# Performance work log

Measured on AMD Instinct MI355X. Metric: run time of the kernel, lower is better.

The kernel has to match this reference:

```python
import jax, jax.numpy as jnp
import numpy as np

B, N, IN_DIM, OUT = 4, 4096, 3, 40
NPTS = [1024, 256, 64, 16]   # base_points // sampling_ratio
K, FIRST_K = 8, 16
EPS = 1e-5

def gelu(t):
    return jax.nn.gelu(t, approximate=False)  # torch nn.GELU default (erf)

def pdist2(a, b):
    # a: (b,d,m), b: (b,d,n) -> squared pairwise distances (b,m,n)
    aa = jnp.sum(a * a, axis=1)[:, :, None]
    bb = jnp.sum(b * b, axis=1)[:, None, :]
    return aa + bb - 2.0 * jnp.einsum('bdm,bdn->bmn', a, b)

def knn_idx(a, b, k):
    # indices of k nearest points of b for each point of a
    return jax.lax.top_k(-pdist2(a, b), k)[1]

def gather_nbr(x, ind):
    # x: (b,d,n), ind: (b,m,k) -> (b,d,m,k)
    b, d, n = x.shape
    m, k = ind.shape[1], ind.shape[2]
    idx = jnp.broadcast_to(ind.reshape(b, 1, m * k), (b, d, m * k))
    return jnp.take_along_axis(x, idx, axis=2).reshape(b, d, m, k)

def bn(x):
    # BatchNorm (training-mode batch stats, gamma=1, beta=0 as at init)
    ax = (0,) + tuple(range(2, x.ndim))
    mu = jnp.mean(x, axis=ax, keepdims=True)
    var = jnp.mean((x - mu) ** 2, axis=ax, keepdims=True)
    return (x - mu) / jnp.sqrt(var + EPS)

def route(x, nbr):
    # (b,d,n),(b,n,k) -> (b,2d,n,k) : cat([neighbor - center, center])
    sel = gather_nbr(x, nbr)
    xc = x[:, :, :, None]
    return jnp.concatenate([sel - xc, jnp.broadcast_to(xc, sel.shape)], axis=1)

def edge_conv(x, l1, l2, sc, k, nbr=None):
    if nbr is None:
        nbr = knn_idx(x, x, k)  # dynamic graph in feature space
    h = jnp.max(jnp.einsum('of,bfnk->bonk', l1, route(x, nbr)), axis=-1)
    h = gelu(bn(h))
    h = jnp.max(jnp.einsum('of,bfnk->bonk', l2, route(h, nbr)), axis=-1)
    short = x if sc is None else jnp.einsum('of,bfn->bon', sc, x)
    return gelu(bn(short + h))

def fps(xyz, m):
    # farthest point sampling; xyz: (b,3,n) -> indices (b,m); start index 0
    pts = jnp.transpose(xyz, (0, 2, 1))  # (b,n,3)
    b, n, _ = pts.shape
    def body(carry, _):
        dmin, last = carry
        lp = jnp.take_along_axis(pts, last[:, None, None], axis=1)  # (b,1,3)
        d = jnp.sum((pts - lp) ** 2, axis=-1)
        dmin = jnp.minimum(dmin, d)
        nxt = jnp.argmax(dmin, axis=-1).astype(jnp.int32)
        return (dmin, nxt), last
    init = (jnp.full((b, n), jnp.inf, pts.dtype), jnp.zeros((b,), jnp.int32))
    _, inds = jax.lax.scan(body, init, None, length=m)
    return jnp.transpose(inds)  # (b,m)

def _forward(x, xyz, mlp_w, mlp_b, c0_l1, c0_l2, l1s, l2s, scs,
             head_w1, head_w2, head_b2):
    b = x.shape[0]
    nbr0 = knn_idx(xyz, xyz, FIRST_K)
    h = gelu(bn(jnp.einsum('oi,bin->bon', mlp_w, x) + mlp_b[None, :, None]))
    h = edge_conv(h, c0_l1, c0_l2, None, FIRST_K, nbr=nbr0)
    cur = xyz
    for i in range(4):
        m = NPTS[i]
        sind = fps(cur, m)
        sxyz = jnp.take_along_axis(
            cur, jnp.broadcast_to(sind[:, None, :], (b, cur.shape[1], m)), axis=2)
        nbr = knn_idx(sxyz, cur, K)
        cur = jnp.mean(gather_nbr(cur, nbr), axis=-1)      # sampled xyz = nbr mean
        h = jnp.max(gather_nbr(h, nbr), axis=-1)           # sampled feat = nbr max
        h = edge_conv(h, l1s[i], l2s[i], scs[i], K)
    g = jnp.mean(h, axis=-1)                               # global average pool
    g = gelu(bn(g @ head_w1.T))
    return g @ head_w2.T + head_b2[None, :]


def setup_inputs() -> dict:
    key = jax.random.key(0)
    ks = jax.random.split(key, 20)
    def w(k, o, i):
        return (jax.random.normal(k, (o, i), jnp.float32) / np.sqrt(i)).astype(jnp.float32)
    return {
        'x': jax.random.normal(ks[0], (B, IN_DIM, N), jnp.float32),
        'xyz': jax.random.normal(ks[1], (B, 3, N), jnp.float32),
        'mlp_w': w(ks[2], 64, IN_DIM), 'mlp_b': jnp.zeros((64,), jnp.float32),
        'c0_l1': w(ks[3], 64, 128), 'c0_l2': w(ks[4], 64, 128),
        's0_l1': w(ks[5], 64, 128), 's0_l2': w(ks[6], 64, 128),
        's1_l1': w(ks[7], 128, 128), 's1_l2': w(ks[8], 128, 256), 's1_sc': w(ks[9], 128, 64),
        's2_l1': w(ks[10], 256, 256), 's2_l2': w(ks[11], 256, 512), 's2_sc': w(ks[12], 256, 128),
        's3_l1': w(ks[13], 512, 512), 's3_l2': w(ks[14], 512, 1024), 's3_sc': w(ks[15], 512, 256),
        'head_w1': w(ks[16], 256, 512), 'head_w2': w(ks[17], OUT, 256),
        'head_b2': jnp.zeros((OUT,), jnp.float32),
    }


def reference(x, xyz, mlp_w, mlp_b, c0_l1, c0_l2, s0_l1, s0_l2,
              s1_l1, s1_l2, s1_sc, s2_l1, s2_l2, s2_sc, s3_l1, s3_l2, s3_sc,
              head_w1, head_w2, head_b2):
    return _forward(x, xyz, mlp_w, mlp_b, c0_l1, c0_l2,
                    (s0_l1, s1_l1, s2_l1, s3_l1),
                    (s0_l2, s1_l2, s2_l2, s3_l2),
                    (None, s1_sc, s2_sc, s3_sc),
                    head_w1, head_w2, head_b2)
```

## Files before the change

kernel.cpp:

```cpp
#include <hip/hip_runtime.h>
#include <math.h>

#define NCHUNK 32
typedef unsigned long long ull;

__device__ __forceinline__ float gelu_f(float v){
  return 0.5f*v*(1.0f+erff(v*0.70710678118654752440f));
}

__device__ __forceinline__ unsigned flipf(float d){
  unsigned u = __float_as_uint(d);
  return (u & 0x80000000u) ? ~u : (u | 0x80000000u);
}

template<int CTRL>
__device__ __forceinline__ ull dpp64(ull k){
  int lo = __builtin_amdgcn_update_dpp(0, (int)(unsigned)k,       CTRL, 0xF, 0xF, true);
  int hi = __builtin_amdgcn_update_dpp(0, (int)(unsigned)(k>>32), CTRL, 0xF, 0xF, true);
  return ((ull)(unsigned)hi<<32) | (unsigned)lo;
}
__device__ __forceinline__ ull rl64(ull k, int l){
  unsigned lo = (unsigned)__builtin_amdgcn_readlane((int)(unsigned)k, l);
  unsigned hi = (unsigned)__builtin_amdgcn_readlane((int)(unsigned)(k>>32), l);
  return ((ull)hi<<32) | lo;
}
__device__ __forceinline__ ull fmax64(ull a, ull b){
  return (ull)__double_as_longlong(fmax(__longlong_as_double((long long)a),
                                        __longlong_as_double((long long)b)));
}
__device__ __forceinline__ ull wave_fmax(ull k){
  k = fmax64(k, dpp64<0xB1>(k));
  k = fmax64(k, dpp64<0x4E>(k));
  k = fmax64(k, dpp64<0x141>(k));
  k = fmax64(k, dpp64<0x140>(k));
  ull a=rl64(k,0), b=rl64(k,16), c=rl64(k,32), d=rl64(k,48);
  return fmax64(fmax64(a,b), fmax64(c,d));
}
template<int CTRL>
__device__ __forceinline__ double dmin_dpp(double k){
  ull o = dpp64<CTRL>((ull)__double_as_longlong(k));
  return fmin(k, __longlong_as_double((long long)o));
}
__device__ __forceinline__ double wave_dmin(double k){
  k = dmin_dpp<0xB1>(k);
  k = dmin_dpp<0x4E>(k);
  k = dmin_dpp<0x141>(k);
  k = dmin_dpp<0x140>(k);
  ull kb = (ull)__double_as_longlong(k);
  double a = __longlong_as_double((long long)rl64(kb,0));
  double b = __longlong_as_double((long long)rl64(kb,16));
  double c = __longlong_as_double((long long)rl64(kb,32));
  double d = __longlong_as_double((long long)rl64(kb,48));
  return fmin(fmin(a,b), fmin(c,d));
}


template<int K, int T>
__device__ __forceinline__ void knn_body(
    const float* __restrict__ cand, int n,
    const float* __restrict__ qsrc, const int* __restrict__ qidx, int m,
    int* __restrict__ nbr, float* __restrict__ outc,
    int b, int qblk, int qoff, char* smem)
{
  float4* tile = (float4*)smem;
  constexpr int NWV = T/64;
  int wv = threadIdx.x >> 6, lane = threadIdx.x & 63;
  int q = qblk*NWV + wv + qoff;
  const float* cb = cand + (size_t)b*3*n;
  int qi = qidx ? qidx[(size_t)b*m + q] : q;
  const float* qb = qsrc + (size_t)b*3*n;
  float qx = qb[qi], qy = qb[n+qi], qz = qb[2*n+qi];
  float aa = (qx*qx + qy*qy) + qz*qz;

  double a[K];
  #pragma unroll
  for (int k=0;k<K;k++) a[k] = 1e300;

  for (int base=0; base<n; base+=1024){
    int cnt = min(1024, n-base);
    for (int j=threadIdx.x; j<cnt; j+=T){
      float x=cb[base+j], y=cb[n+base+j], z=cb[2*n+base+j];
      tile[j] = make_float4(x,y,z,(x*x+y*y)+z*z);
    }
    __syncthreads();
    int steps = cnt >> 6;
    double jd = (double)(base + lane);
    for (int i=0;i<steps;i++){
      int j = lane + (i<<6);
      float4 c = tile[j];
      float d = aa + c.w - 2.0f*((qx*c.x+qy*c.y)+qz*c.z);
      double key = (double)flipf(d) * 4096.0 + jd;
      if (key < a[K-1]){
        #pragma unroll
        for (int k=K-1;k>=1;k--)
          a[k] = fmin(fmax(a[k-1], key), a[k]);
        a[0] = fmin(a[0], key);
      }
      jd += 64.0;
    }
    __syncthreads();
  }

  double head = a[0];
  int res[K];
  #pragma unroll
  for (int r=0; r<K; r++){
    double mk = wave_dmin(head);
    res[r] = (int)((ull)mk & 4095u);
    if (head == mk){
      #pragma unroll
      for (int i2=0;i2<K-1;i2++) a[i2]=a[i2+1];
      a[K-1] = 1e300;
      head = a[0];
    }
  }
  if (lane == 0){
    int* o = nbr + ((size_t)b*m + q)*K;
    #pragma unroll
    for (int r=0;r<K;r++) o[r] = res[r];
  }
  if (outc != nullptr && lane < 3){
    const float* cd = cb + (size_t)lane*n;
    float s=0;
    #pragma unroll
    for (int k=0;k<K;k++) s += cd[res[k]];
    outc[((size_t)b*3 + lane)*m + q] = s * (1.0f/K);
  }
}

template<int K>
__device__ __forceinline__ void topk_body(
    const float* __restrict__ G, const float* __restrict__ aa, int m,
    int* __restrict__ nbr, int b, int qblk, char* smem)
{
  float* abs_s = (float*)smem;
  int wv = threadIdx.x >> 6, lane = threadIdx.x & 63;
  int q = qblk*4 + wv;
  const float* ab = aa + (size_t)b*m;
  for (int j=threadIdx.x; j<m; j+=256) abs_s[j] = ab[j];
  __syncthreads();
  float aq = ab[q];
  const float* Gq = G + ((size_t)b*m + q)*m;

  double a[K];
  #pragma unroll
  for (int k=0;k<K;k++) a[k] = 1e300;

  int steps = (m+63)>>6;
  double jd = (double)lane;
  for (int i=0;i<steps;i++){
    int j = lane + (i<<6);
    double key = 1e300;
    if (j < m){
      float g = Gq[j];
      float d = aq + abs_s[j] - 2.0f*g;
      key = (double)flipf(d) * 4096.0 + jd;
    }
    if (key < a[K-1]){
      #pragma unroll
      for (int k=K-1;k>=1;k--)
        a[k] = fmin(fmax(a[k-1], key), a[k]);
      a[0] = fmin(a[0], key);
    }
    jd += 64.0;
  }
  double head = a[0];
  int res[K];
  #pragma unroll
  for (int r=0; r<K; r++){
    double mk = wave_dmin(head);
    res[r] = (int)((ull)mk & 4095u);
    if (head == mk){
      #pragma unroll
      for (int i2=0;i2<K-1;i2++) a[i2]=a[i2+1];
      a[K-1] = 1e300;
      head = a[0];
    }
  }
  if (lane == 0){
    int* o = nbr + ((size_t)b*m + q)*K;
    #pragma unroll
    for (int r=0;r<K;r++) o[r] = res[r];
  }
}

template<int NP, int T, int M>
__device__ __forceinline__ void fps_mw_seg(const float* __restrict__ cur, int n,
                                           int* __restrict__ sind, float* __restrict__ gdmin,
                                           int b, int M0, int M1, char* smem)
{
  constexpr int NW = T/64;
  int tid = threadIdx.x;
  int wv = tid>>6;
  const float* cb = cur + (size_t)b*3*n;
  float4* lp = (float4*)smem;
  ull* wred = (ull*)(smem + sizeof(float4)*NP*T);
  float* gd = gdmin + (size_t)b*n;
  float px[NP], py[NP], pz[NP], dmin[NP];
  unsigned nj[NP];
  #pragma unroll
  for (int s=0;s<NP;s++){
    int j = tid + s*T;
    px[s]=cb[j]; py[s]=cb[n+j]; pz[s]=cb[2*n+j];
    dmin[s] = (M0==0) ? 1e30f : gd[j];
    nj[s] = (unsigned)(~j);
    lp[j] = make_float4(px[s],py[s],pz[s],0.f);
  }
  __syncthreads();
  int ci = (M0==0) ? 0 : sind[(size_t)b*M + (M0-1)];
  float4 w0 = lp[ci];
  float X = w0.x, Y = w0.y, Z = w0.z;
  if (M0==0 && tid==0) sind[(size_t)b*M] = 0;
  __builtin_amdgcn_s_setprio(3);
  int p = 0;
  int s0 = (M0==0) ? 1 : M0;
  for (int step=s0; step<M1; step++){
    ull key[NP];
    #pragma unroll
    for (int s=0;s<NP;s++){
      float dx=px[s]-X, dy=py[s]-Y, dz=pz[s]-Z;
      float d = (dx*dx + dy*dy) + dz*dz;
      float nd = fminf(dmin[s], d);
      dmin[s] = nd;
      key[s] = ((ull)__float_as_uint(nd)<<32) | nj[s];
    }
    #pragma unroll
    for (int w=NP; w>1; w>>=1)
      #pragma unroll
      for (int i=0;i<NP;i++) if (i < (w>>1))
        key[i] = fmax64(key[i], key[i+(w>>1)]);
    ull wk = wave_fmax(key[0]);
    if ((tid&63)==0) wred[p*NW + wv] = wk;
    __syncthreads();
    const ulonglong2* wp2 = (const ulonglong2*)(wred + p*NW);
    ulonglong2 m0 = wp2[0], m1 = wp2[1], m2 = wp2[2], m3 = wp2[3];
    ull gk = fmax64(fmax64(fmax64(m0.x,m0.y), fmax64(m1.x,m1.y)),
                    fmax64(fmax64(m2.x,m2.y), fmax64(m3.x,m3.y)));
    int gi = (int)(~(unsigned)gk);
    if (tid==0) sind[(size_t)b*M + step] = gi;
    float4 wp = lp[gi];
    X=wp.x; Y=wp.y; Z=wp.z;
    p ^= 1;
  }
  __builtin_amdgcn_s_setprio(0);
  #pragma unroll
  for (int s=0;s<NP;s++) gd[tid + s*T] = dmin[s];
}

template<int NP, int M>
__device__ __forceinline__ void fps_sw_body(const float* __restrict__ cur, int n,
                                            int* __restrict__ sind, int b, char* smem)
{
  int lane = threadIdx.x;
  const float* cb = cur + (size_t)b*3*n;
  float4* lp = (float4*)smem;
  float px[NP], py[NP], pz[NP], dmin[NP];
  unsigned nj[NP];
  #pragma unroll
  for (int s=0;s<NP;s++){
    int j = lane + s*64;
    px[s]=cb[j]; py[s]=cb[n+j]; pz[s]=cb[2*n+j]; dmin[s]=1e30f;
    nj[s] = (unsigned)(~j);
    lp[j] = make_float4(px[s],py[s],pz[s],0.f);
  }
  float X = lp[0].x, Y = lp[0].y, Z = lp[0].z;
  if (lane==0) sind[(size_t)b*M] = 0;
  __builtin_amdgcn_s_setprio(3);
  for (int step=1; step<M; step++){
    ull key[NP];
    #pragma unroll
    for (int s=0;s<NP;s++){
      float dx=px[s]-X, dy=py[s]-Y, dz=pz[s]-Z;
      float d = (dx*dx + dy*dy) + dz*dz;
      float nd = fminf(dmin[s], d);
      dmin[s] = nd;
      key[s] = ((ull)__float_as_uint(nd)<<32) | nj[s];
    }
    #pragma unroll
    for (int w=NP; w>1; w>>=1)
      #pragma unroll
      for (int i=0;i<NP;i++) if (i < (w>>1))
        key[i] = fmax64(key[i], key[i+(w>>1)]);
    ull gk = wave_fmax(key[0]);
    int gi = (int)(~(unsigned)gk);
    if (lane==0) sind[(size_t)b*M + step] = gi;
    float4 wp = lp[gi];
    X=wp.x; Y=wp.y; Z=wp.z;
  }
  __builtin_amdgcn_s_setprio(0);
}

template<int NP, int M>
__device__ __forceinline__ void fps_sw_seg(const float* __restrict__ cur, int n,
                                           int* __restrict__ sind, float* __restrict__ gdmin,
                                           int b, int M0, int M1, char* smem)
{
  int lane = threadIdx.x;
  const float* cb = cur + (size_t)b*3*n;
  float4* lp = (float4*)smem;
  float* gd = gdmin + (size_t)b*n;
  float px[NP], py[NP], pz[NP], dmin[NP];
  unsigned nj[NP];
  #pragma unroll
  for (int s=0;s<NP;s++){
    int j = lane + s*64;
    px[s]=cb[j]; py[s]=cb[n+j]; pz[s]=cb[2*n+j];
    dmin[s] = (M0==0) ? 1e30f : gd[j];
    nj[s] = (unsigned)(~j);
    lp[j] = make_float4(px[s],py[s],pz[s],0.f);
  }
  int ci = (M0==0) ? 0 : sind[(size_t)b*M + (M0-1)];
  float4 w0 = lp[ci];
  float X = w0.x, Y = w0.y, Z = w0.z;
  if (M0==0 && lane==0) sind[(size_t)b*M] = 0;
  __builtin_amdgcn_s_setprio(3);
  int s0 = (M0==0) ? 1 : M0;
  for (int step=s0; step<M1; step++){
    ull key[NP];
    #pragma unroll
    for (int s=0;s<NP;s++){
      float dx=px[s]-X, dy=py[s]-Y, dz=pz[s]-Z;
      float d = (dx*dx + dy*dy) + dz*dz;
      float nd = fminf(dmin[s], d);
      dmin[s] = nd;
      key[s] = ((ull)__float_as_uint(nd)<<32) | nj[s];
    }
    #pragma unroll
    for (int w=NP; w>1; w>>=1)
      #pragma unroll
      for (int i=0;i<NP;i++) if (i < (w>>1))
        key[i] = fmax64(key[i], key[i+(w>>1)]);
    ull gk = wave_fmax(key[0]);
    int gi = (int)(~(unsigned)gk);
    if (lane==0) sind[(size_t)b*M + step] = gi;
    float4 wp = lp[gi];
    X=wp.x; Y=wp.y; Z=wp.z;
  }
  __builtin_amdgcn_s_setprio(0);
  #pragma unroll
  for (int s=0;s<NP;s++) gd[lane + s*64] = dmin[s];
}

template<bool DUAL, bool BN>
__device__ __forceinline__ void gemm_body(
    const float* __restrict__ A, const float* __restrict__ B,
    float* __restrict__ out0, float* __restrict__ out1,
    int M, int N, int Kd, int lda, int ldb, int ldo, int boff,
    long sA, long sB, long sO, const float* __restrict__ part, float invR,
    int bxi, int byi, int bzi, char* smem)
{
  A += (size_t)bzi * sA; B += (size_t)bzi * sB;
  float* o0 = out0 + (size_t)bzi * sO;
  float* o1 = DUAL ? (out1 + (size_t)bzi * sO) : nullptr;
  int rowBase = byi*64, colBase = bxi*64;
  float (*As)[64]  = (float(*)[64])smem;
  float (*Bs0)[64] = (float(*)[64])(smem + 4096);
  float (*Bs1)[64] = (float(*)[64])(smem + 8192);
  float* mu_s = (float*)(smem + 12288);
  float* var_s = mu_s + 512;
  int tid = threadIdx.x;
  if (BN){
    for (int oo=tid; oo<Kd; oo+=blockDim.x){
      float s=0, q=0;
      #pragma unroll 4
      for (int c=0;c<NCHUNK;c++){
        s += part[(size_t)c*1024 + oo];
        q += part[(size_t)(NCHUNK+c)*1024 + oo];
      }
      float mu = s*invR;
      mu_s[oo] = mu;
      var_s[oo] = q*invR - mu*mu;
    }
    __syncthreads();
  }
  int ty = tid>>4, tx = tid&15;
  float acc0[4][4] = {}, acc1[4][4] = {};
  int lr = tid>>2, lk = (tid&3)*4;
  for (int k0=0; k0<Kd; k0+=16) {
    float4 va = make_float4(0,0,0,0);
    int r = rowBase + lr;
    if (r < M) va = *(const float4*)(A + (size_t)r*lda + k0 + lk);
    if (BN){
      int c = k0 + lk;
      va.x = gelu_f((va.x - mu_s[c+0]) / sqrtf(var_s[c+0] + 1e-5f));
      va.y = gelu_f((va.y - mu_s[c+1]) / sqrtf(var_s[c+1] + 1e-5f));
      va.z = gelu_f((va.z - mu_s[c+2]) / sqrtf(var_s[c+2] + 1e-5f));
      va.w = gelu_f((va.w - mu_s[c+3]) / sqrtf(var_s[c+3] + 1e-5f));
    }
    As[lk+0][lr]=va.x; As[lk+1][lr]=va.y; As[lk+2][lr]=va.z; As[lk+3][lr]=va.w;
    float4 vb = make_float4(0,0,0,0), vb2 = make_float4(0,0,0,0);
    int c2 = colBase + lr;
    if (c2 < N) {
      vb = *(const float4*)(B + (size_t)c2*ldb + k0 + lk);
      if (DUAL) vb2 = *(const float4*)(B + (size_t)c2*ldb + boff + k0 + lk);
    }
    Bs0[lk+0][lr]=vb.x; Bs0[lk+1][lr]=vb.y; Bs0[lk+2][lr]=vb.z; Bs0[lk+3][lr]=vb.w;
    if (DUAL) {
      Bs1[lk+0][lr]=vb2.x-vb.x; Bs1[lk+1][lr]=vb2.y-vb.y;
      Bs1[lk+2][lr]=vb2.z-vb.z; Bs1[lk+3][lr]=vb2.w-vb.w;
    }
    __syncthreads();
    #pragma unroll
    for (int kk=0;kk<16;kk++){
      float4 a  = *(const float4*)&As[kk][ty*4];
      float4 b0 = *(const float4*)&Bs0[kk][tx*4];
      float av[4]={a.x,a.y,a.z,a.w};
      float b0v[4]={b0.x,b0.y,b0.z,b0.w};
      #pragma unroll
      for (int i=0;i<4;i++)
        #pragma unroll
        for (int j=0;j<4;j++) acc0[i][j] = fmaf(av[i], b0v[j], acc0[i][j]);
      if (DUAL) {
        float4 b1 = *(const float4*)&Bs1[kk][tx*4];
        float b1v[4]={b1.x,b1.y,b1.z,b1.w};
        #pragma unroll
        for (int i=0;i<4;i++)
          #pragma unroll
          for (int j=0;j<4;j++) acc1[i][j] = fmaf(av[i], b1v[j], acc1[i][j]);
      }
    }
    __syncthreads();
  }
  #pragma unroll
  for (int i=0;i<4;i++){
    int r = rowBase + ty*4 + i;
    if (r < M) {
      #pragma unroll
      for (int j=0;j<4;j++){
        int c = colBase + tx*4 + j;
        if (c < N) {
          o0[(size_t)r*ldo + c] = acc0[i][j];
          if (DUAL) o1[(size_t)r*ldo + c] = acc1[i][j];
        }
      }
    }
  }
}

template<bool DUAL, bool BN>
__device__ __forceinline__ void gemm_body_g(
    const float* __restrict__ A, const float* __restrict__ B,
    float* __restrict__ out0, float* __restrict__ out1,
    int M, int N, int Kd, int lda, int ldb, int ldo, int boff,
    const float* __restrict__ part, float invR,
    int bxi, int byi, char* smem)
{
  int rowBase = byi*64, colBase = bxi*64;
  float (*As)[64]  = (float(*)[64])smem;
  float (*Bs0)[64] = (float(*)[64])(smem + 4096);
  float (*Bs1)[64] = (float(*)[64])(smem + 8192);
  float* mu_s = (float*)(smem + 12288);
  float* var_s = mu_s + 512;
  int tid = threadIdx.x;
  bool act = tid < 256;
  if (BN){
    for (int oo=tid; oo<Kd; oo+=blockDim.x){
      float s=0, q=0;
      #pragma unroll 4
      for (int c=0;c<NCHUNK;c++){
        s += part[(size_t)c*1024 + oo];
        q += part[(size_t)(NCHUNK+c)*1024 + oo];
      }
      float mu = s*invR;
      mu_s[oo] = mu;
      var_s[oo] = q*invR - mu*mu;
    }
    __syncthreads();
  }
  int ty = tid>>4, tx = tid&15;
  float acc0[4][4] = {}, acc1[4][4] = {};
  int lr = tid>>2, lk = (tid&3)*4;
  for (int k0=0; k0<Kd; k0+=16) {
    if (act){
      float4 va = make_float4(0,0,0,0);
      int r = rowBase + lr;
      if (r < M) va = *(const float4*)(A + (size_t)r*lda + k0 + lk);
      if (BN){
        int c = k0 + lk;
        va.x = gelu_f((va.x - mu_s[c+0]) / sqrtf(var_s[c+0] + 1e-5f));
        va.y = gelu_f((va.y - mu_s[c+1]) / sqrtf(var_s[c+1] + 1e-5f));
        va.z = gelu_f((va.z - mu_s[c+2]) / sqrtf(var_s[c+2] + 1e-5f));
        va.w = gelu_f((va.w - mu_s[c+3]) / sqrtf(var_s[c+3] + 1e-5f));
      }
      As[lk+0][lr]=va.x; As[lk+1][lr]=va.y; As[lk+2][lr]=va.z; As[lk+3][lr]=va.w;
      float4 vb = make_float4(0,0,0,0), vb2 = make_float4(0,0,0,0);
      int c2 = colBase + lr;
      if (c2 < N) {
        vb = *(const float4*)(B + (size_t)c2*ldb + k0 + lk);
        if (DUAL) vb2 = *(const float4*)(B + (size_t)c2*ldb + boff + k0 + lk);
      }
      Bs0[lk+0][lr]=vb.x; Bs0[lk+1][lr]=vb.y; Bs0[lk+2][lr]=vb.z; Bs0[lk+3][lr]=vb.w;
      if (DUAL) {
        Bs1[lk+0][lr]=vb2.x-vb.x; Bs1[lk+1][lr]=vb2.y-vb.y;
        Bs1[lk+2][lr]=vb2.z-vb.z; Bs1[lk+3][lr]=vb2.w-vb.w;
      }
    }
    __syncthreads();
    if (act){
      #pragma unroll
      for (int kk=0;kk<16;kk++){
        float4 a  = *(const float4*)&As[kk][ty*4];
        float4 b0 = *(const float4*)&Bs0[kk][tx*4];
        float av[4]={a.x,a.y,a.z,a.w};
        float b0v[4]={b0.x,b0.y,b0.z,b0.w};
        #pragma unroll
        for (int i=0;i<4;i++)
          #pragma unroll
          for (int j=0;j<4;j++) acc0[i][j] = fmaf(av[i], b0v[j], acc0[i][j]);
        if (DUAL) {
          float4 b1 = *(const float4*)&Bs1[kk][tx*4];
          float b1v[4]={b1.x,b1.y,b1.z,b1.w};
          #pragma unroll
          for (int i=0;i<4;i++)
            #pragma unroll
            for (int j=0;j<4;j++) acc1[i][j] = fmaf(av[i], b1v[j], acc1[i][j]);
        }
      }
    }
    __syncthreads();
  }
  if (act){
    #pragma unroll
    for (int i=0;i<4;i++){
      int r = rowBase + ty*4 + i;
      if (r < M) {
        #pragma unroll
        for (int j=0;j<4;j++){
          int c = colBase + tx*4 + j;
          if (c < N) {
            out0[(size_t)r*ldo + c] = acc0[i][j];
            if (DUAL) out1[(size_t)r*ldo + c] = acc1[i][j];
          }
        }
      }
    }
  }
}

__device__ __forceinline__ void gather_elem(
    const float* __restrict__ P, const int* __restrict__ nbr,
    const float* __restrict__ addA, const float* __restrict__ addB,
    float* __restrict__ out, int n_out, int n_src, int O, int K, int total, int e)
{
  if (e >= total) return;
  int o = e % O; int r = e / O;
  int b = r / n_out; int i = r % n_out;
  const int* nb = nbr + ((size_t)b*n_out + i)*K;
  float mx = -1e38f;
  for (int k=0;k<K;k++){
    int j = nb[k];
    float v = P[((size_t)b*n_src + j)*O + o];
    mx = fmaxf(mx, v);
  }
  float res = mx;
  if (addA) res += addA[e];
  if (addB) res = addB[e] + res;
  out[e] = res;
}

__device__ __forceinline__ void gatherbn_body(
    const float* __restrict__ P, const int* __restrict__ nbr,
    const float* __restrict__ part, float invR,
    float* __restrict__ out, float* __restrict__ aa,
    int n_out, int n_src, int O, int K, int blk, char* smem)
{
  float* mu_s = (float*)smem; float* var_s = mu_s + 256; float* sv = var_s + 256;
  int tid = threadIdx.x;
  for (int oo=tid; oo<O; oo+=256){
    float s=0, q=0;
    #pragma unroll 4
    for (int c=0;c<NCHUNK;c++){
      s += part[(size_t)c*1024 + oo];
      q += part[(size_t)(NCHUNK+c)*1024 + oo];
    }
    float mu = s*invR;
    mu_s[oo] = mu;
    var_s[oo] = q*invR - mu*mu;
  }
  __syncthreads();
  int e = blk*256 + tid;
  int o = e % O; int r = e / O;
  int b = r / n_out; int i = r % n_out;
  const int* nb = nbr + ((size_t)b*n_out + i)*K;
  float mu = mu_s[o], sd = sqrtf(var_s[o] + 1e-5f);
  float mx = -1e38f;
  for (int k=0;k<K;k++){
    int j = nb[k];
    float p = P[((size_t)b*n_src + j)*O + o];
    float v = gelu_f((p - mu)/sd);
    mx = fmaxf(mx, v);
  }
  out[e] = mx;
  sv[tid] = mx*mx;
  __syncthreads();
  for (int st=O>>1; st>0; st>>=1){
    if (o < st) sv[tid] += sv[tid+st];
    __syncthreads();
  }
  if (o == 0) aa[r] = sv[tid];
}


#define FPS_SMEM 65664

__global__ __launch_bounds__(512,2) void mega1(
    const float* __restrict__ xyz, const float* __restrict__ x,
    const float* __restrict__ mlpw, const float* __restrict__ mlpb,
    int* __restrict__ sind0, float* __restrict__ gdmin,
    int* __restrict__ nbr0, float* __restrict__ hA, int M0, int M1)
{
  __shared__ __align__(16) char SMEM[FPS_SMEM];
  int bid = blockIdx.x;
  if (bid < 4){
    fps_mw_seg<8,512,1024>(xyz, 4096, sind0, gdmin, bid, M0, M1, SMEM);
  } else if (bid < 4+2048){
    int kb = bid - 4;
    knn_body<16,512>(xyz, 4096, xyz, nullptr, 4096, nbr0, nullptr, kb>>9, kb&511, 0, SMEM);
  } else {
    int e = (bid - 2052)*512 + threadIdx.x;
    if (e < 4*4096*64){
      int o = e & 63; int r = e >> 6;
      int b = r / 4096; int i = r % 4096;
      const float* xb = x + (size_t)b*3*4096;
      hA[e] = ((mlpw[o*3+0]*xb[i] + mlpw[o*3+1]*xb[4096+i]) + mlpw[o*3+2]*xb[2*4096+i]) + mlpb[o];
    }
  }
}

__global__ __launch_bounds__(512,2) void fps_bngelu(
    const float* fcur, int* sind, float* gdmin, int M0, int M1,
    float* __restrict__ xx, const float* __restrict__ part, float invR, int O, int total)
{
  __shared__ __align__(16) char SMEM[FPS_SMEM];
  if (blockIdx.x < 4){
    fps_mw_seg<8,512,1024>(fcur, 4096, sind, gdmin, blockIdx.x, M0, M1, SMEM);
    return;
  }
  float* mu_s = (float*)SMEM; float* var_s = mu_s + 512;
  for (int oo=threadIdx.x; oo<O; oo+=512){
    float s=0, q=0;
    #pragma unroll 4
    for (int c=0;c<NCHUNK;c++){
      s += part[(size_t)c*1024 + oo];
      q += part[(size_t)(NCHUNK+c)*1024 + oo];
    }
    float mu = s*invR;
    mu_s[oo] = mu;
    var_s[oo] = q*invR - mu*mu;
  }
  __syncthreads();
  int e = (blockIdx.x-4)*512 + threadIdx.x;
  if (e >= total) return;
  int o = e % O;
  float v = (xx[e]-mu_s[o]) / sqrtf(var_s[o] + 1e-5f);
  xx[e] = gelu_f(v);
}

template<bool DUAL, bool BN>
__global__ __launch_bounds__(512,2) void fps0_gemm(
    const float* fcur, int* sind, float* gdmin, int M0, int M1,
    const float* A, const float* B, float* out0, float* out1,
    int Mg, int Ng, int Kd, int lda, int ldb, int ldo, int boff,
    const float* part, float invR, int nbx)
{
  __shared__ __align__(16) char SMEM[FPS_SMEM];
  if (blockIdx.x < 4){
    fps_mw_seg<8,512,1024>(fcur, 4096, sind, gdmin, blockIdx.x, M0, M1, SMEM);
    return;
  }
  int l = blockIdx.x - 4;
  gemm_body_g<DUAL,BN>(A,B,out0,out1,Mg,Ng,Kd,lda,ldb,ldo,boff,part,invR, l%nbx, l/nbx, SMEM);
}

__global__ __launch_bounds__(512,2) void fps0_gather_knn(
    const float* fcur, int* sind, float* gdmin, int M0, int M1,
    const float* cand, int n, const float* qsrc, const int* qidx, int m,
    int* nbrOut, float* outc, int KNB,
    const float* P, const int* nbr, const float* addA, const float* addB,
    float* out, int n_out, int n_src, int O, int K, int total)
{
  __shared__ __align__(16) char SMEM[FPS_SMEM];
  if (blockIdx.x < 4){
    fps_mw_seg<8,512,1024>(fcur, 4096, sind, gdmin, blockIdx.x, M0, M1, SMEM);
    return;
  }
  int l = blockIdx.x - 4;
  if (l < KNB){
    knn_body<8,512>(cand, n, qsrc, qidx, m, nbrOut, outc, l>>6, l&63, 0, SMEM);
    return;
  }
  int e = (l-KNB)*512 + threadIdx.x;
  gather_elem(P, nbr, addA, addB, out, n_out, n_src, O, K, total, e);
}

__global__ __launch_bounds__(512,2) void fps0_gather(
    const float* fcur, int* sind, float* gdmin, int M0, int M1,
    const float* P, const int* nbr, const float* addA, const float* addB,
    float* out, int n_out, int n_src, int O, int K, int total)
{
  __shared__ __align__(16) char SMEM[FPS_SMEM];
  if (blockIdx.x < 4){
    fps_mw_seg<8,512,1024>(fcur, 4096, sind, gdmin, blockIdx.x, M0, M1, SMEM);
    return;
  }
  int e = (blockIdx.x-4)*512 + threadIdx.x;
  gather_elem(P, nbr, addA, addB, out, n_out, n_src, O, K, total, e);
}

__global__ __launch_bounds__(512,2) void fps0_stats(
    const float* fcur, int* sind, float* gdmin, int M0, int M1,
    const float* __restrict__ x, int R, int O, float* __restrict__ part)
{
  __shared__ __align__(16) char SMEM[FPS_SMEM];
  if (blockIdx.x < 4){
    fps_mw_seg<8,512,1024>(fcur, 4096, sind, gdmin, blockIdx.x, M0, M1, SMEM);
    return;
  }
  int o = threadIdx.x;
  if (o >= O) return;
  int chunk = blockIdx.x - 4;
  int per = (R + NCHUNK - 1)/NCHUNK;
  int r0 = chunk*per, r1 = min(r0+per, R);
  float s=0, q=0;
  for (int r=r0; r<r1; r++){ float v = x[(size_t)r*O + o]; s+=v; q+=v*v; }
  part[(size_t)chunk*1024 + o] = s;
  part[(size_t)(NCHUNK+chunk)*1024 + o] = q;
}

__global__ __launch_bounds__(256) void knn_wave8(
    const float* cand, int n, const float* qsrc, const int* qidx, int m, int qoff,
    int* nbr, float* outc)
{
  __shared__ __align__(16) char SMEM[16384];
  knn_body<8,256>(cand, n, qsrc, qidx, m, nbr, outc, blockIdx.y, blockIdx.x, qoff, SMEM);
}

__global__ __launch_bounds__(256) void fps1_gatherbn(
    const float* fcur, int* sind, float* gdmin, int M0, int M1,
    const float* P, const int* nbr, const float* part, float invR,
    float* out, float* aa, int n_out, int n_src, int O, int K)
{
  __shared__ __align__(16) char SMEM[16384];
  if (blockIdx.x < 4){
    if (threadIdx.x < 64) fps_sw_seg<16,256>(fcur, 1024, sind, gdmin, blockIdx.x, M0, M1, SMEM);
    return;
  }
  gatherbn_body(P, nbr, part, invR, out, aa, n_out, n_src, O, K, blockIdx.x-4, SMEM);
}

__global__ __launch_bounds__(256) void fps1_gram(
    const float* fcur, int* sind, float* gdmin, int M0, int M1,
    const float* Ag, float* outg, int Mg, int Kg, long sAg, long sOg, int ngx, int ngy)
{
  __shared__ __align__(16) char SMEM[16896];
  if (blockIdx.x < 4){
    if (threadIdx.x < 64) fps_sw_seg<16,256>(fcur, 1024, sind, gdmin, blockIdx.x, M0, M1, SMEM);
    return;
  }
  int l = blockIdx.x - 4;
  int bx = l % ngx, by = (l/ngx) % ngy, bz = l/(ngx*ngy);
  gemm_body<false,false>(Ag,Ag,outg,nullptr,Mg,Mg,Kg,Kg,Kg,Mg,0,sAg,sAg,sOg,nullptr,0.f,bx,by,bz,SMEM);
}

__global__ __launch_bounds__(256) void fps1_topk(
    const float* fcur, int* sind, float* gdmin, int M0, int M1,
    const float* G, const float* aa, int m, int* nbr)
{
  __shared__ __align__(16) char SMEM[16384];
  if (blockIdx.x < 4){
    if (threadIdx.x < 64) fps_sw_seg<16,256>(fcur, 1024, sind, gdmin, blockIdx.x, M0, M1, SMEM);
    return;
  }
  int l = blockIdx.x - 4;
  int qpb = m/4;
  topk_body<8>(G, aa, m, nbr, l/qpb, l%qpb, SMEM);
}

template<int NP, int M>
__global__ __launch_bounds__(256) void fps_gather(
    const float* fcur, int fn, int* sind,
    const float* P, const int* nbr, const float* addA, const float* addB,
    float* out, int n_out, int n_src, int O, int K, int total)
{
  __shared__ __align__(16) char SMEM[(NP*64*16 > 4096) ? NP*64*16 : 4096];
  if (blockIdx.x < 4){
    if (threadIdx.x < 64) fps_sw_body<NP,M>(fcur, fn, sind, blockIdx.x, SMEM);
    return;
  }
  gather_elem(P, nbr, addA, addB, out, n_out, n_src, O, K, total, (blockIdx.x-4)*256 + threadIdx.x);
}

template<bool DUAL, bool BN>
__global__ __launch_bounds__(256) void knn_gemm2(
    const float* cand, int n, const float* qsrc, const int* qidx, int m,
    int* nbrOut, float* outc, int KNB,
    const float* A, const float* B, float* out0, float* out1,
    int Mg, int Ng, int Kd, int boff,
    const float* part, float invR, int nbx)
{
  __shared__ __align__(16) char SMEM[16896];
  if (blockIdx.x < KNB){
    int qpb = m/4;
    knn_body<8,256>(cand, n, qsrc, qidx, m, nbrOut, outc, blockIdx.x/qpb, blockIdx.x%qpb, 0, SMEM);
    return;
  }
  int l = blockIdx.x - KNB;
  gemm_body<DUAL,BN>(A,B,out0,out1,Mg,Ng,Kd,Kd,DUAL?2*Kd:Kd,Ng,boff,0,0,0,part,invR, l%nbx, l/nbx, 0, SMEM);
}

__global__ __launch_bounds__(256) void knn_gatherbn(
    const float* cand, int n, const float* qsrc, const int* qidx, int m,
    int* nbrOut, int KNB,
    const float* P, const int* nbr, const float* part, float invR,
    float* out, float* aa, int n_out, int n_src, int O, int K)
{
  __shared__ __align__(16) char SMEM[16384];
  if (blockIdx.x < KNB){
    int qpb = m/4;
    knn_body<8,256>(cand, n, qsrc, qidx, m, nbrOut, nullptr, blockIdx.x/qpb, blockIdx.x%qpb, 0, SMEM);
    return;
  }
  gatherbn_body(P, nbr, part, invR, out, aa, n_out, n_src, O, K, blockIdx.x-KNB, SMEM);
}

__global__ __launch_bounds__(256) void gram_gemm(
    const float* Ag, float* outg, int Mg, int Kg, long sAg, long sOg,
    int ngx, int ngy, int NG,
    const float* A2, const float* B2, float* o20, float* o21,
    int M2, int N2, int K2, int boff2, int nb2x)
{
  __shared__ __align__(16) char SMEM[16896];
  int l = blockIdx.x;
  if (l < NG){
    int bx = l % ngx, by = (l/ngx) % ngy, bz = l/(ngx*ngy);
    gemm_body<false,false>(Ag,Ag,outg,nullptr,Mg,Mg,Kg,Kg,Kg,Mg,0,sAg,sAg,sOg,nullptr,0.f,bx,by,bz,SMEM);
    return;
  }
  l -= NG;
  gemm_body<true,false>(A2,B2,o20,o21,M2,N2,K2,K2,2*K2,N2,boff2,0,0,0,nullptr,0.f, l%nb2x, l/nb2x, 0, SMEM);
}

__global__ __launch_bounds__(256) void gemm2sc(
    const float* A2, const float* B2, float* o20, float* o21, int R, int O2, int O1v,
    const float* part, float invR,
    const float* Asc, const float* Bsc, float* osc, int Cin,
    int nbx, int nby)
{
  __shared__ __align__(16) char SMEM[16896];
  int l = blockIdx.x;
  int half = nbx*nby;
  if (l < half){
    gemm_body<true,true>(A2,B2,o20,o21,R,O2,O1v,O1v,2*O1v,O2,O1v,0,0,0,part,invR, l%nbx, l/nbx, 0, SMEM);
  } else {
    l -= half;
    gemm_body<false,false>(Asc,Bsc,osc,nullptr,R,O2,Cin,Cin,Cin,O2,0,0,0,0,nullptr,0.f, l%nbx, l/nbx, 0, SMEM);
  }
}

__global__ __launch_bounds__(256) void gathermax_kernel(
    const float* P, const int* nbr, const float* addA, const float* addB,
    float* out, int n_out, int n_src, int O, int K, int total)
{
  gather_elem(P, nbr, addA, addB, out, n_out, n_src, O, K, total, blockIdx.x*256 + threadIdx.x);
}

__global__ __launch_bounds__(256) void gatherbn_kernel(
    const float* P, const int* nbr, const float* part, float invR,
    float* out, float* aa, int n_out, int n_src, int O, int K)
{
  __shared__ __align__(16) char SMEM[3072];
  gatherbn_body(P, nbr, part, invR, out, aa, n_out, n_src, O, K, blockIdx.x, SMEM);
}

template<int K>
__global__ __launch_bounds__(256) void topk_wave(
    const float* __restrict__ G, const float* __restrict__ aa, int m,
    int* __restrict__ nbr)
{
  __shared__ __align__(16) char SMEM[4096];
  topk_body<K>(G, aa, m, nbr, blockIdx.y, blockIdx.x, SMEM);
}

__global__ void stats_part_kernel(const float* __restrict__ x, int R, int O,
                                  float* __restrict__ part)
{
  int o = threadIdx.x;
  int chunk = blockIdx.x;
  int per = (R + NCHUNK - 1)/NCHUNK;
  int r0 = chunk*per, r1 = min(r0+per, R);
  float s=0, q=0;
  for (int r=r0; r<r1; r++){ float v = x[(size_t)r*O + o]; s+=v; q+=v*v; }
  part[(size_t)chunk*1024 + o] = s;
  part[(size_t)(NCHUNK+chunk)*1024 + o] = q;
}

__global__ __launch_bounds__(1024) void head_kernel(const float* __restrict__ h,
    const float* __restrict__ part, float invR,
    const float* __restrict__ w1, const float* __restrict__ w2,
    const float* __restrict__ b2, float* __restrict__ out)
{
  __shared__ __align__(16) float mu_s[512], var_s[512];
  __shared__ __align__(16) float g[4*512];
  __shared__ __align__(16) float t[4*256];
  int tid = threadIdx.x;
  for (int oo=tid; oo<512; oo+=1024){
    float s=0, q=0;
    #pragma unroll 4
    for (int c=0;c<NCHUNK;c++){
      s += part[(size_t)c*1024 + oo];
      q += part[(size_t)(NCHUNK+c)*1024 + oo];
    }
    float mu = s*invR;
    mu_s[oo] = mu;
    var_s[oo] = q*invR - mu*mu;
  }
  __syncthreads();
  for (int e=tid; e<2048; e+=1024){
    int b=e>>9, c=e&511;
    float mu = mu_s[c], sd = sqrtf(var_s[c] + 1e-5f);
    float s=0;
    for (int p=0;p<16;p++){
      float v = h[((size_t)(b*16+p))*512 + c];
      s += gelu_f((v-mu)/sd);
    }
    g[e] = s * (1.0f/16.0f);
  }
  __syncthreads();
  {
    int b = tid>>8, j = tid&255;
    const float4* gr = (const float4*)(g + b*512);
    const float4* wr = (const float4*)(w1 + (size_t)j*512);
    float s=0;
    for (int c=0;c<128;c++){
      float4 a=gr[c], w=wr[c];
      s = fmaf(a.x,w.x, fmaf(a.y,w.y, fmaf(a.z,w.z, fmaf(a.w,w.w, s))));
    }
    t[tid] = s;
  }
  __syncthreads();
  if (tid < 256){
    float v0=t[tid], v1=t[256+tid], v2=t[512+tid], v3=t[768+tid];
    float mu = ((v0+v1)+v2+v3)*0.25f;
    float d0=v0-mu, d1=v1-mu, d2=v2-mu, d3=v3-mu;
    float var = ((d0*d0+d1*d1)+d2*d2+d3*d3)*0.25f;
    float sq = sqrtf(var + 1e-5f);
    t[tid]     = gelu_f(d0/sq);
    t[256+tid] = gelu_f(d1/sq);
    t[512+tid] = gelu_f(d2/sq);
    t[768+tid] = gelu_f(d3/sq);
  }
  __syncthreads();
  if (tid < 160){
    int b = tid/40, o = tid%40;
    const float* tr = t + b*256; const float* wr = w2 + (size_t)o*256;
    float s=0;
    for (int j=0;j<256;j++) s = fmaf(tr[j], wr[j], s);
    out[tid] = s + b2[o];
  }
}

extern "C" void kernel_launch(void* const* d_in, const int* in_sizes, int n_in,
                              void* d_out, int out_size, void* d_ws, size_t ws_size,
                              hipStream_t stream)
{
  const float* x    = (const float*)d_in[0];
  const float* xyz  = (const float*)d_in[1];
  const float* mlpw = (const float*)d_in[2];
  const float* mlpb = (const float*)d_in[3];
  const float* c0l1 = (const float*)d_in[4];
  const float* c0l2 = (const float*)d_in[5];
  const float* L1[4] = {(const float*)d_in[6], (const float*)d_in[8],
                        (const float*)d_in[11], (const float*)d_in[14]};
  const float* L2[4] = {(const float*)d_in[7], (const float*)d_in[9],
                        (const float*)d_in[12], (const float*)d_in[15]};
  const float* SC[4] = {nullptr, (const float*)d_in[10],
                        (const float*)d_in[13], (const float*)d_in[16]};
  const float* hw1 = (const float*)d_in[17];
  const float* hw2 = (const float*)d_in[18];
  const float* hb2 = (const float*)d_in[19];
  float* out = (float*)d_out;

  float* ws = (float*)d_ws;
  const size_t MF = 1024*1024;
  float* D    = ws;
  float* hA   = ws + 4*MF;
  float* hX   = ws + 5*MF;
  float* hP   = ws + 6*MF;
  float* hCT  = ws + 7*MF;
  float* hSH  = ws + 8*MF;
  float* hH1  = ws + 9*MF;
  float* hOUT = ws + 10*MF;
  float* aux  = ws + 11*MF;
  int*   nbr0  = (int*)aux;                 aux += 262144;
  int*   nbrS0 = (int*)aux;                 aux += 32768;
  int*   nbrS1 = (int*)aux;                 aux += 8192;
  int*   nbrS2 = (int*)aux;                 aux += 2048;
  int*   nbrS3 = (int*)aux;                 aux += 512;
  int*   nbrF  = (int*)aux;                 aux += 32768;
  int*   sind0 = (int*)aux;                 aux += 4096;
  int*   sind1 = (int*)aux;                 aux += 1024;
  int*   sind2 = (int*)aux;                 aux += 256;
  int*   sind3 = (int*)aux;                 aux += 64;
  float* aa    = aux;                       aux += 4096;
  float* cur1  = aux;                       aux += 12288;
  float* cur2  = aux;                       aux += 3072;
  float* cur3  = aux;                       aux += 768;
  float* part  = aux;                       aux += 65536;
  float* gdmin = aux;                       aux += 16384;

  int tot0 = 4*4096*64;

  mega1<<<4100, 512, 0, stream>>>(xyz, x, mlpw, mlpb, sind0, gdmin, nbr0, hA, 0, 260);
  stats_part_kernel<<<NCHUNK, 64, 0, stream>>>(hA, 16384, 64, part);
  fps_bngelu<<<4+2048, 512, 0, stream>>>(xyz, sind0, gdmin, 260, 390, hA, part, 1.0f/16384.0f, 64, tot0);
  fps0_gemm<true,false><<<4+256, 512, 0, stream>>>(xyz, sind0, gdmin, 390, 517,
      hA, c0l1, hP, hCT, 16384, 64, 64, 64, 128, 64, 64, nullptr, 0.f, 1);
  fps0_gather_knn<<<4+256+2048, 512, 0, stream>>>(xyz, sind0, gdmin, 517, 644,
      xyz, 4096, xyz, sind0, 1024, nbrS0, cur1, 256,
      hP, nbr0, hCT, nullptr, hH1, 4096, 4096, 64, 16, 1048576);
  stats_part_kernel<<<NCHUNK, 64, 0, stream>>>(hH1, 16384, 64, part);
  fps0_gemm<true,true><<<4+256, 512, 0, stream>>>(xyz, sind0, gdmin, 644, 771,
      hH1, c0l2, hP, hCT, 16384, 64, 64, 64, 128, 64, 64, part, 1.0f/16384.0f, 1);
  fps0_gather<<<4+2048, 512, 0, stream>>>(xyz, sind0, gdmin, 771, 898,
      hP, nbr0, hCT, hA, hOUT, 4096, 4096, 64, 16, 1048576);
  fps0_stats<<<4+NCHUNK, 512, 0, stream>>>(xyz, sind0, gdmin, 898, 1024,
      hOUT, 16384, 64, part);

  knn_wave8<<<dim3(128,4),256,0,stream>>>(xyz, 4096, xyz, sind0, 1024, 512, nbrS0, cur1);

  fps1_gatherbn<<<4+1024,256,0,stream>>>(cur1, sind1, gdmin, 0, 86,
      hOUT, nbrS0, part, 1.0f/16384.0f, hX, aa, 1024, 4096, 64, 8);
  fps1_gram<<<4+1024,256,0,stream>>>(cur1, sind1, gdmin, 86, 171,
      hX, D, 1024, 64, (long)1024*64, (long)1024*1024, 16, 16);
  fps1_topk<<<4+1024,256,0,stream>>>(cur1, sind1, gdmin, 171, 256,
      D, aa, 1024, nbrF);
  knn_gemm2<true,false><<<256+64,256,0,stream>>>(cur1, 1024, cur1, sind1, 256,
      nbrS1, cur2, 256,
      hX, L1[0], hP, hCT, 4096, 64, 64, 64, nullptr, 0.f, 1);
  fps_gather<4,64><<<4+1024,256,0,stream>>>(cur2, 256, sind2,
      hP, nbrF, hCT, nullptr, hH1, 1024, 1024, 64, 8, 262144);
  stats_part_kernel<<<NCHUNK, 64, 0, stream>>>(hH1, 4096, 64, part);
  knn_gemm2<true,true><<<64+64,256,0,stream>>>(cur2, 256, cur2, sind2, 64,
      nbrS2, cur3, 64,
      hH1, L2[0], hP, hCT, 4096, 64, 64, 64, part, 1.0f/4096.0f, 1);
  fps_gather<1,16><<<4+1024,256,0,stream>>>(cur3, 64, sind3,
      hP, nbrF, hCT, hX, hA, 1024, 1024, 64, 8, 262144);
  stats_part_kernel<<<NCHUNK, 64, 0, stream>>>(hA, 4096, 64, part);
  knn_gatherbn<<<16+256,256,0,stream>>>(cur3, 64, cur3, sind3, 16,
      nbrS3, 16,
      hA, nbrS1, part, 1.0f/4096.0f, hX, aa, 256, 1024, 64, 8);

  const int   mArr[3]   = {256, 64, 16};
  const int   nsrcArr[3]= {1024, 256, 64};
  const int   CinArr[3] = {64, 128, 256};
  const int   OArr[3]   = {128, 256, 512};
  const int*  nbrSs[3]  = {nbrS1, nbrS2, nbrS3};
  float* hcur = hA;
  float invRprev = 1.0f/4096.0f;
  for (int s=0;s<3;s++){
    int m = mArr[s], nsrc = nsrcArr[s], Cin = CinArr[s], O1 = OArr[s], O2 = OArr[s];
    int R = 4*m;
    int th = R*Cin;
    if (s > 0){
      gatherbn_kernel<<<th/256,256,0,stream>>>(hcur, nbrSs[s], part, invRprev,
                                               hX, aa, m, nsrc, Cin, 8);
    }
    int ngx = (m+63)/64, ngy = (m+63)/64;
    int NG = ngx*ngy*4;
    int nb1x = (O1+63)/64, nb1y = (R+63)/64;
    gram_gemm<<<NG + nb1x*nb1y, 256, 0, stream>>>(
        hX, D, m, Cin, (long)m*Cin, (long)m*m, ngx, ngy, NG,
        hX, L1[s+1], hP, hCT, R, O1, Cin, Cin, nb1x);
    topk_wave<8><<<dim3(m/4,4),256,0,stream>>>(D, aa, m, nbrF);
    int t1 = R*O1;
    gathermax_kernel<<<(t1+255)/256,256,0,stream>>>(hP, nbrF, hCT, nullptr, hH1, m, m, O1, 8, t1);
    stats_part_kernel<<<NCHUNK, O1, 0, stream>>>(hH1, R, O1, part);
    int nbx = (O2+63)/64, nby = (R+63)/64;
    gemm2sc<<<2*nbx*nby,256,0,stream>>>(hH1, L2[s+1], hP, hCT, R, O2, O1, part, 1.0f/R,
                                        hX, SC[s+1], hSH, Cin, nbx, nby);
    int t2 = R*O2;
    float* outbuf = (s&1) ? hA : hOUT;
    gathermax_kernel<<<(t2+255)/256,256,0,stream>>>(hP, nbrF, hCT, hSH, outbuf, m, m, O2, 8, t2);
    stats_part_kernel<<<NCHUNK, O2, 0, stream>>>(outbuf, R, O2, part);
    hcur = outbuf;
    invRprev = 1.0f/R;
  }

  head_kernel<<<1,1024,0,stream>>>(hcur, part, 1.0f/64.0f, hw1, hw2, hb2, out);
}
```

Before: 1.553 ms.

## Spread stage-0 kNN query blocks across FPS-overlapped kernels and split gather-BN

The standalone stage-0 kNN kernel is removed. Its query blocks are spread across the existing FPS-carrying launches: gemm, gather and stats now each run an extra slice of kNN blocks alongside the FPS segment. The FPS iteration ranges per kernel are rebalanced to match. The remaining kNN queries are fused with part of the gather-BN work into a new tail kernel, and fps1_gatherbn handles only the leftover gather-BN blocks. The aim is to fill idle CUs while the serial FPS runs, at the cost of more complex block indexing and a risk of load imbalance.

```diff
diff --git a/kernel.cpp b/kernel.cpp
--- a/kernel.cpp
+++ b/kernel.cpp
@@ -657,8 +657,10 @@
 }
 
 template<bool DUAL, bool BN>
-__global__ __launch_bounds__(512,2) void fps0_gemm(
+__global__ __launch_bounds__(512,2) void fps0_gemm_knn(
     const float* fcur, int* sind, float* gdmin, int M0, int M1,
+    const float* cand, int n, const float* qsrc, const int* qidx, int m,
+    int* nbrOut, float* outc, int qoff, int NQB, int KNB,
     const float* A, const float* B, float* out0, float* out1,
     int Mg, int Ng, int Kd, int lda, int ldb, int ldo, int boff,
     const float* part, float invR, int nbx)
@@ -669,13 +671,18 @@
     return;
   }
   int l = blockIdx.x - 4;
+  if (l < KNB){
+    knn_body<8,512>(cand, n, qsrc, qidx, m, nbrOut, outc, l/NQB, l%NQB, qoff, SMEM);
+    return;
+  }
+  l -= KNB;
   gemm_body_g<DUAL,BN>(A,B,out0,out1,Mg,Ng,Kd,lda,ldb,ldo,boff,part,invR, l%nbx, l/nbx, SMEM);
 }
 
 __global__ __launch_bounds__(512,2) void fps0_gather_knn(
     const float* fcur, int* sind, float* gdmin, int M0, int M1,
     const float* cand, int n, const float* qsrc, const int* qidx, int m,
-    int* nbrOut, float* outc, int KNB,
+    int* nbrOut, float* outc, int qoff, int NQB, int KNB,
     const float* P, const int* nbr, const float* addA, const float* addB,
     float* out, int n_out, int n_src, int O, int K, int total)
 {
@@ -686,39 +693,32 @@
   }
   int l = blockIdx.x - 4;
   if (l < KNB){
-    knn_body<8,512>(cand, n, qsrc, qidx, m, nbrOut, outc, l>>6, l&63, 0, SMEM);
+    knn_body<8,512>(cand, n, qsrc, qidx, m, nbrOut, outc, l/NQB, l%NQB, qoff, SMEM);
     return;
   }
   int e = (l-KNB)*512 + threadIdx.x;
   gather_elem(P, nbr, addA, addB, out, n_out, n_src, O, K, total, e);
 }
 
-__global__ __launch_bounds__(512,2) void fps0_gather(
+__global__ __launch_bounds__(512,2) void fps0_stats_knn(
     const float* fcur, int* sind, float* gdmin, int M0, int M1,
-    const float* P, const int* nbr, const float* addA, const float* addB,
-    float* out, int n_out, int n_src, int O, int K, int total)
+    const float* cand, int n, const float* qsrc, const int* qidx, int m,
+    int* nbrOut, float* outc, int qoff, int NQB, int KNB,
+    const float* __restrict__ x, int R, int O, float* __restrict__ part)
 {
   __shared__ __align__(16) char SMEM[FPS_SMEM];
   if (blockIdx.x < 4){
     fps_mw_seg<8,512,1024>(fcur, 4096, sind, gdmin, blockIdx.x, M0, M1, SMEM);
     return;
   }
-  int e = (blockIdx.x-4)*512 + threadIdx.x;
-  gather_elem(P, nbr, addA, addB, out, n_out, n_src, O, K, total, e);
-}
-
-__global__ __launch_bounds__(512,2) void fps0_stats(
-    const float* fcur, int* sind, float* gdmin, int M0, int M1,
-    const float* __restrict__ x, int R, int O, float* __restrict__ part)
-{
-  __shared__ __align__(16) char SMEM[FPS_SMEM];
-  if (blockIdx.x < 4){
-    fps_mw_seg<8,512,1024>(fcur, 4096, sind, gdmin, blockIdx.x, M0, M1, SMEM);
+  int l = blockIdx.x - 4;
+  if (l < KNB){
+    knn_body<8,512>(cand, n, qsrc, qidx, m, nbrOut, outc, l/NQB, l%NQB, qoff, SMEM);
     return;
   }
   int o = threadIdx.x;
   if (o >= O) return;
-  int chunk = blockIdx.x - 4;
+  int chunk = l - KNB;
   int per = (R + NCHUNK - 1)/NCHUNK;
   int r0 = chunk*per, r1 = min(r0+per, R);
   float s=0, q=0;
@@ -727,12 +727,21 @@
   part[(size_t)(NCHUNK+chunk)*1024 + o] = q;
 }
 
-__global__ __launch_bounds__(256) void knn_wave8(
-    const float* cand, int n, const float* qsrc, const int* qidx, int m, int qoff,
-    int* nbr, float* outc)
+__global__ __launch_bounds__(256) void knn_gatherbn_tail(
+    const float* cand, int n, const float* qsrc, const int* qidx, int m,
+    int* nbrOut, float* outc, int qoff, int NQB, int KNB,
+    const float* P, const int* nbr, const float* part, float invR,
+    float* out, float* aa, int n_out, int n_src, int O, int K)
 {
   __shared__ __align__(16) char SMEM[16384];
-  knn_body<8,256>(cand, n, qsrc, qidx, m, nbr, outc, blockIdx.y, blockIdx.x, qoff, SMEM);
+  if (blockIdx.x < KNB){
+    int l = blockIdx.x;
+    knn_body<8,256>(cand, n, qsrc, qidx, m, nbrOut, outc, l/NQB, l%NQB, qoff, SMEM);
+    return;
+  }
+  int l = blockIdx.x - KNB;
+  int blk = (l/196)*256 + (l%196);
+  gatherbn_body(P, nbr, part, invR, out, aa, n_out, n_src, O, K, blk, SMEM);
 }
 
 __global__ __launch_bounds__(256) void fps1_gatherbn(
@@ -745,7 +754,9 @@
     if (threadIdx.x < 64) fps_sw_seg<16,256>(fcur, 1024, sind, gdmin, blockIdx.x, M0, M1, SMEM);
     return;
   }
-  gatherbn_body(P, nbr, part, invR, out, aa, n_out, n_src, O, K, blockIdx.x-4, SMEM);
+  int l = blockIdx.x - 4;
+  int blk = (l/60)*256 + 196 + (l%60);
+  gatherbn_body(P, nbr, part, invR, out, aa, n_out, n_src, O, K, blk, SMEM);
 }
 
 __global__ __launch_bounds__(256) void fps1_gram(
@@ -1010,29 +1021,34 @@
 
   int tot0 = 4*4096*64;
 
-  mega1<<<4100, 512, 0, stream>>>(xyz, x, mlpw, mlpb, sind0, gdmin, nbr0, hA, 0, 260);
+  mega1<<<4100, 512, 0, stream>>>(xyz, x, mlpw, mlpb, sind0, gdmin, nbr0, hA, 0, 300);
   stats_part_kernel<<<NCHUNK, 64, 0, stream>>>(hA, 16384, 64, part);
-  fps_bngelu<<<4+2048, 512, 0, stream>>>(xyz, sind0, gdmin, 260, 390, hA, part, 1.0f/16384.0f, 64, tot0);
-  fps0_gemm<true,false><<<4+256, 512, 0, stream>>>(xyz, sind0, gdmin, 390, 517,
+  fps_bngelu<<<4+2048, 512, 0, stream>>>(xyz, sind0, gdmin, 300, 345, hA, part, 1.0f/16384.0f, 64, tot0);
+  fps0_gemm_knn<true,false><<<4+128+256, 512, 0, stream>>>(xyz, sind0, gdmin, 345, 470,
+      xyz, 4096, xyz, sind0, 1024, nbrS0, cur1, 0, 32, 128,
       hA, c0l1, hP, hCT, 16384, 64, 64, 64, 128, 64, 64, nullptr, 0.f, 1);
-  fps0_gather_knn<<<4+256+2048, 512, 0, stream>>>(xyz, sind0, gdmin, 517, 644,
-      xyz, 4096, xyz, sind0, 1024, nbrS0, cur1, 256,
+  fps0_gather_knn<<<4+104+2048, 512, 0, stream>>>(xyz, sind0, gdmin, 470, 645,
+      xyz, 4096, xyz, sind0, 1024, nbrS0, cur1, 256, 26, 104,
       hP, nbr0, hCT, nullptr, hH1, 4096, 4096, 64, 16, 1048576);
   stats_part_kernel<<<NCHUNK, 64, 0, stream>>>(hH1, 16384, 64, part);
-  fps0_gemm<true,true><<<4+256, 512, 0, stream>>>(xyz, sind0, gdmin, 644, 771,
+  fps0_gemm_knn<true,true><<<4+88+256, 512, 0, stream>>>(xyz, sind0, gdmin, 645, 720,
+      xyz, 4096, xyz, sind0, 1024, nbrS0, cur1, 464, 22, 88,
       hH1, c0l2, hP, hCT, 16384, 64, 64, 64, 128, 64, 64, part, 1.0f/16384.0f, 1);
-  fps0_gather<<<4+2048, 512, 0, stream>>>(xyz, sind0, gdmin, 771, 898,
+  fps0_gather_knn<<<4+24+2048, 512, 0, stream>>>(xyz, sind0, gdmin, 720, 820,
+      xyz, 4096, xyz, sind0, 1024, nbrS0, cur1, 640, 6, 24,
       hP, nbr0, hCT, hA, hOUT, 4096, 4096, 64, 16, 1048576);
-  fps0_stats<<<4+NCHUNK, 512, 0, stream>>>(xyz, sind0, gdmin, 898, 1024,
+  fps0_stats_knn<<<4+48+NCHUNK, 512, 0, stream>>>(xyz, sind0, gdmin, 820, 1024,
+      xyz, 4096, xyz, sind0, 1024, nbrS0, cur1, 688, 12, 48,
       hOUT, 16384, 64, part);
 
-  knn_wave8<<<dim3(128,4),256,0,stream>>>(xyz, 4096, xyz, sind0, 1024, 512, nbrS0, cur1);
-
-  fps1_gatherbn<<<4+1024,256,0,stream>>>(cur1, sind1, gdmin, 0, 86,
+  knn_gatherbn_tail<<<240+784, 256, 0, stream>>>(
+      xyz, 4096, xyz, sind0, 1024, nbrS0, cur1, 784, 60, 240,
       hOUT, nbrS0, part, 1.0f/16384.0f, hX, aa, 1024, 4096, 64, 8);
-  fps1_gram<<<4+1024,256,0,stream>>>(cur1, sind1, gdmin, 86, 171,
+  fps1_gatherbn<<<4+240, 256, 0, stream>>>(cur1, sind1, gdmin, 0, 86,
+      hOUT, nbrS0, part, 1.0f/16384.0f, hX, aa, 1024, 4096, 64, 8);
+  fps1_gram<<<4+1024, 256, 0, stream>>>(cur1, sind1, gdmin, 86, 171,
       hX, D, 1024, 64, (long)1024*64, (long)1024*1024, 16, 16);
-  fps1_topk<<<4+1024,256,0,stream>>>(cur1, sind1, gdmin, 171, 256,
+  fps1_topk<<<4+1024, 256, 0, stream>>>(cur1, sind1, gdmin, 171, 256,
       D, aa, 1024, nbrF);
   knn_gemm2<true,false><<<256+64,256,0,stream>>>(cur1, 1024, cur1, sind1, 256,
       nbrS1, cur2, 256,
```

Result: faster. 1.500 ms (-3.5%).
